# Performance work log

Measured on AMD Instinct MI355X. Metric: run time of the kernel, lower is better.

The kernel has to match this reference:

```python
import jax, jax.numpy as jnp
import numpy as np

N = 20000        # nodes
E = 320000       # edges
F_IN = 512       # feature_size
H = 512          # hidden_dim (z dim)
OUT = 1024       # output_size


def setup_inputs() -> dict:
    key = jax.random.key(0)
    ks = jax.random.split(key, 24)
    p = lambda k, shape: jax.random.normal(k, shape, jnp.float32) * 0.02
    return {
        "x": jax.random.normal(ks[0], (N, F_IN), jnp.float32),
        "edge_index": jax.random.randint(ks[1], (2, E), 0, N),
        "edge_weight": jax.random.uniform(ks[2], (E,), dtype=jnp.float32),
        "beta": jnp.float32(1.0),
        "y_target": jax.random.uniform(ks[3], (1,), dtype=jnp.float32),
        "eps": jax.random.normal(ks[4], (N, H), jnp.float32),
        # GCNConv weights (in_dim, out_dim) + bias
        "W1": p(ks[5], (F_IN, 1024)), "b1": jnp.zeros((1024,), jnp.float32),
        "W2": p(ks[6], (1024, 512)), "b2": jnp.zeros((512,), jnp.float32),
        "W3": p(ks[7], (512, 256)),  "b3": jnp.zeros((256,), jnp.float32),
        # VAE heads
        "Wmu": p(ks[8], (256, H)),  "bmu": jnp.zeros((H,), jnp.float32),
        "Wlv": p(ks[9], (256, H)),  "blv": jnp.zeros((H,), jnp.float32),
        # decoder MLP: (2H+1) -> (2H+1) -> OUT
        "Wd1": p(ks[10], (2 * H + 1, 2 * H + 1)), "bd1": jnp.zeros((2 * H + 1,), jnp.float32),
        "Wd2": p(ks[11], (2 * H + 1, OUT)),       "bd2": jnp.zeros((OUT,), jnp.float32),
    }


def gcn_conv(x, W, b, src, dst, ew):
    # PyG GCNConv: add self-loops (weight 1), symmetric deg normalization,
    # aggregate normalized neighbor messages of x @ W, then add bias.
    xw = x @ W                                             # [N, out]
    deg = jax.ops.segment_sum(ew, dst, num_segments=N) + 1.0
    dinv = jax.lax.rsqrt(deg)                              # [N]
    norm = dinv[src] * ew * dinv[dst]                      # [E]
    agg = jax.ops.segment_sum(norm[:, None] * xw[src], dst, num_segments=N)
    return agg + (dinv * dinv)[:, None] * xw + b


def l2norm(x):
    n = jnp.sqrt(jnp.sum(x * x, axis=1, keepdims=True))
    return x / jnp.maximum(n, 1e-12)


def reference(x, edge_index, edge_weight, beta, y_target, eps,
              W1, b1, W2, b2, W3, b3, Wmu, bmu, Wlv, blv, Wd1, bd1, Wd2, bd2):
    src, dst = edge_index[0], edge_index[1]
    h = jax.nn.relu(l2norm(gcn_conv(x, W1, b1, src, dst, edge_weight)))
    h = jax.nn.relu(l2norm(gcn_conv(h, W2, b2, src, dst, edge_weight)))
    h = jax.nn.relu(l2norm(gcn_conv(h, W3, b3, src, dst, edge_weight)))
    mu = h @ Wmu + bmu                                     # [N, H]
    logvar = h @ Wlv + blv                                 # [N, H]
    # reparameterize(mu, beta * logvar) with eps ~ 0.01 * N(0,1)
    std = jnp.exp(0.5 * beta * logvar)
    z = mu + (0.01 * eps) * std                            # [N, H]
    out1 = jnp.max(z, axis=0, keepdims=True)               # global max pool [1, H]
    out2 = jnp.mean(z, axis=0, keepdims=True)              # global mean pool [1, H]
    reduce_z = jnp.concatenate([out1, out2, y_target[:, None]], axis=-1)  # [1, 2H+1]
    hdec = jax.nn.relu(reduce_z @ Wd1 + bd1)
    recon_x = jax.nn.sigmoid(hdec @ Wd2 + bd2)             # [1, OUT]
    return (recon_x, mu, logvar)
```

## Files before the change

### kernel.cpp

```cpp
#include <hip/hip_runtime.h>

#define NN 20000
#define EE 320000
#define MPAD 20096
#define MTILES 157
#define DKB 128
#define DCH 9

typedef unsigned short u16;
typedef unsigned int u32;
typedef __attribute__((ext_vector_type(8))) short short8;
typedef __attribute__((ext_vector_type(4))) float f32x4;

__device__ inline float bf16lo(u32 u) { return __uint_as_float(u << 16); }
__device__ inline float bf16hi(u32 u) { return __uint_as_float(u & 0xffff0000u); }
__device__ inline u16 f2b(float f) {
  u32 u = __float_as_uint(f);
  u += 0x7fffu + ((u >> 16) & 1u);
  return (u16)(u >> 16);
}
__device__ inline u32 pack2(float a, float b) {
  return (u32)f2b(a) | ((u32)f2b(b) << 16);
}

__device__ inline void gload16(const void* g, void* l) {
  __builtin_amdgcn_global_load_lds(
      (const __attribute__((address_space(1))) void*)g,
      (__attribute__((address_space(3))) void*)l, 16, 0, 0);
}

__device__ inline int xcd_ord(int wg, int nwg) {
  int q = nwg >> 3, r = nwg & 7;
  int xcd = wg & 7, k = wg >> 3;
  return xcd * q + min(xcd, r) + k;
}

__global__ void k_zeroi(int* __restrict__ p, int n) {
  int i = blockIdx.x * blockDim.x + threadIdx.x;
  if (i < n) p[i] = 0;
}

__global__ void k_f2b2(const float* __restrict__ in, u16* __restrict__ out, int npairs) {
  for (int i = blockIdx.x * blockDim.x + threadIdx.x; i < npairs; i += gridDim.x * blockDim.x) {
    float2 v = *(const float2*)(in + 2 * i);
    ((u32*)out)[i] = pack2(v.x, v.y);
  }
}

__global__ void k_wt_all(const float* __restrict__ W1, const float* __restrict__ W2,
                         const float* __restrict__ W3, const float* __restrict__ Wmu,
                         const float* __restrict__ Wlv,
                         u16* __restrict__ T1, u16* __restrict__ T2,
                         u16* __restrict__ T3, u16* __restrict__ Tmu,
                         u16* __restrict__ Tlv) {
  int b = blockIdx.x;
  const float* W; u16* T; int K, N;
  if (b < 2048)      { W = W1;  T = T1;  K = 512;  N = 1024; }
  else if (b < 4096) { W = W2;  T = T2;  K = 1024; N = 512;  b -= 2048; }
  else if (b < 4608) { W = W3;  T = T3;  K = 512;  N = 256;  b -= 4096; }
  else if (b < 5120) { W = Wmu; T = Tmu; K = 256;  N = 512;  b -= 4608; }
  else               { W = Wlv; T = Tlv; K = 256;  N = 512;  b -= 5120; }
  int kb = K >> 8;
  int n = b / kb;
  int k = (b % kb) * 256 + threadIdx.x;
  T[(size_t)n * K + k] = f2b(W[(size_t)k * N + n]);
}

__global__ void k_count(const int* __restrict__ ei, int* __restrict__ counts) {
  int e = blockIdx.x * blockDim.x + threadIdx.x;
  if (e < EE) atomicAdd(counts + ei[EE + e], 1);
}

__global__ __launch_bounds__(256)
void k_scan(const int* __restrict__ counts, int* __restrict__ rowptr, int* __restrict__ cursor) {
  const int CHUNK = (NN + 255) / 256;
  int t = threadIdx.x;
  int lo = t * CHUNK, hi = min(lo + CHUNK, NN);
  int s = 0;
  for (int i = lo; i < hi; ++i) s += counts[i];
  __shared__ int tsum[256];
  tsum[t] = s;
  __syncthreads();
  if (t == 0) {
    int run = 0;
    for (int i = 0; i < 256; ++i) { int v = tsum[i]; tsum[i] = run; run += v; }
  }
  __syncthreads();
  int run = tsum[t];
  for (int i = lo; i < hi; ++i) {
    rowptr[i] = run;
    cursor[i] = run;
    run += counts[i];
  }
  if (t == 255) rowptr[NN] = EE;
}

__global__ void k_fill(const int* __restrict__ ei, const float* __restrict__ ew,
                       int* __restrict__ cursor, int* __restrict__ colsrc,
                       float* __restrict__ ecw) {
  int e = blockIdx.x * blockDim.x + threadIdx.x;
  if (e < EE) {
    int d = ei[EE + e];
    int pos = atomicAdd(cursor + d, 1);
    colsrc[pos] = ei[e];
    ecw[pos] = ew[e];
  }
}

__global__ void k_degcsr(const int* __restrict__ rowptr, const float* __restrict__ ecw,
                         float* __restrict__ dinv, float* __restrict__ dinv2) {
  int i = blockIdx.x * blockDim.x + threadIdx.x;
  if (i < NN) {
    float s = 0.f;
    for (int e = rowptr[i]; e < rowptr[i + 1]; ++e) s += ecw[e];
    float d = s + 1.0f;
    dinv[i] = rsqrtf(d);
    dinv2[i] = 1.0f / d;
  }
}

template <bool STORE_BF16, bool HAS_BIAS>
__global__ __launch_bounds__(256)
void k_mfma(const u16* __restrict__ A, const u16* __restrict__ BT,
            const float* __restrict__ bias, void* __restrict__ C,
            int M, int K, int N) {
  __shared__ u16 Asm[2][128 * 32];
  __shared__ u16 Bsm[2][128 * 32];
  const int tid = threadIdx.x;
  const int ntn = N >> 7;
  int ord = xcd_ord(blockIdx.x, gridDim.x);
  const int m0 = (ord / ntn) * 128;
  const int n0 = (ord % ntn) * 128;
  const int lane = tid & 63;
  const int wave = tid >> 6;
  const int wm = (wave >> 1) * 64;
  const int wn = (wave & 1) * 64;
  const int qm = lane & 15;
  const int quad = lane >> 4;

  f32x4 acc[4][4];
#pragma unroll
  for (int i = 0; i < 4; ++i)
#pragma unroll
    for (int j = 0; j < 4; ++j) acc[i][j] = (f32x4){0.f, 0.f, 0.f, 0.f};

  const int row_s = tid >> 2, kc_s = (tid & 3) * 8;

#pragma unroll
  for (int h = 0; h < 2; ++h) {
    int row = h * 64 + row_s;
    gload16(A + (size_t)(m0 + row) * K + kc_s, Asm[0] + row * 32 + kc_s);
    gload16(BT + (size_t)(n0 + row) * K + kc_s, Bsm[0] + row * 32 + kc_s);
  }
  __syncthreads();

  const int nk = K >> 5;
  int cur = 0;
  for (int t = 0; t < nk; ++t) {
    if (t + 1 < nk) {
      int k1 = (t + 1) * 32;
#pragma unroll
      for (int h = 0; h < 2; ++h) {
        int row = h * 64 + row_s;
        gload16(A + (size_t)(m0 + row) * K + k1 + kc_s, Asm[cur ^ 1] + row * 32 + kc_s);
        gload16(BT + (size_t)(n0 + row) * K + k1 + kc_s, Bsm[cur ^ 1] + row * 32 + kc_s);
      }
    }
    short8 af[4], bfr[4];
#pragma unroll
    for (int i = 0; i < 4; ++i)
      af[i] = *(const short8*)(Asm[cur] + (wm + i * 16 + qm) * 32 + quad * 8);
#pragma unroll
    for (int j = 0; j < 4; ++j)
      bfr[j] = *(const short8*)(Bsm[cur] + (wn + j * 16 + qm) * 32 + quad * 8);
#pragma unroll
    for (int i = 0; i < 4; ++i)
#pragma unroll
      for (int j = 0; j < 4; ++j)
        acc[i][j] = __builtin_amdgcn_mfma_f32_16x16x32_bf16(af[i], bfr[j], acc[i][j], 0, 0, 0);
    if (t + 1 < nk) {
      __syncthreads();
      cur ^= 1;
    }
  }

#pragma unroll
  for (int i = 0; i < 4; ++i) {
#pragma unroll
    for (int r = 0; r < 4; ++r) {
      int row = m0 + wm + i * 16 + quad * 4 + r;
      if (row >= M) continue;
#pragma unroll
      for (int j = 0; j < 4; ++j) {
        int col = n0 + wn + j * 16 + qm;
        float v = acc[i][j][r];
        if (HAS_BIAS) v += bias[col];
        if (STORE_BF16) ((u16*)C)[(size_t)row * N + col] = f2b(v);
        else ((float*)C)[(size_t)row * N + col] = v;
      }
    }
  }
}

__global__ __launch_bounds__(256, 3)
void k_heads(const u16* __restrict__ A, const u16* __restrict__ BmuT,
             const u16* __restrict__ BlvT, const float* __restrict__ bmu,
             const float* __restrict__ blv, const float* __restrict__ eps,
             const float* __restrict__ beta_p, float* __restrict__ mu_out,
             float* __restrict__ lv_out, float* __restrict__ pmax,
             float* __restrict__ psum) {
  const int K = 256;
  __shared__ float smemf[4352];
  u16* Asm = (u16*)smemf;
  u16* Bmu = (u16*)((char*)smemf + 8192);
  u16* Blv = (u16*)((char*)smemf + 12288);
  float* stmu = smemf;
  float* stlv = smemf + 32 * 68;
  const int tid = threadIdx.x;
  int ord = xcd_ord(blockIdx.x, gridDim.x);
  const int mt = ord >> 3;
  const int m0 = mt * 128;
  const int n0 = (ord & 7) * 64;
  const int lane = tid & 63;
  const int wave = tid >> 6;
  const int wm = (wave >> 1) * 64;
  const int wn = (wave & 1) * 32;
  const int qm = lane & 15;
  const int quad = lane >> 4;

  f32x4 am[4][2], al[4][2];
#pragma unroll
  for (int i = 0; i < 4; ++i)
#pragma unroll
    for (int j = 0; j < 2; ++j) {
      am[i][j] = (f32x4){0.f, 0.f, 0.f, 0.f};
      al[i][j] = (f32x4){0.f, 0.f, 0.f, 0.f};
    }

  for (int k0 = 0; k0 < K; k0 += 32) {
#pragma unroll
    for (int h = 0; h < 2; ++h) {
      int c = h * 256 + tid;
      int row = c >> 2, kc = c & 3;
      gload16(A + (size_t)(m0 + row) * K + k0 + kc * 8, Asm + c * 8);
    }
    {
      int row = tid >> 2, kc = tid & 3;
      gload16(BmuT + (size_t)(n0 + row) * K + k0 + kc * 8, Bmu + tid * 8);
      gload16(BlvT + (size_t)(n0 + row) * K + k0 + kc * 8, Blv + tid * 8);
    }
    __syncthreads();
    short8 af[4], bm[2], bl[2];
#pragma unroll
    for (int i = 0; i < 4; ++i)
      af[i] = *(const short8*)(Asm + (wm + i * 16 + qm) * 32 + quad * 8);
#pragma unroll
    for (int j = 0; j < 2; ++j) {
      bm[j] = *(const short8*)(Bmu + (wn + j * 16 + qm) * 32 + quad * 8);
      bl[j] = *(const short8*)(Blv + (wn + j * 16 + qm) * 32 + quad * 8);
    }
#pragma unroll
    for (int i = 0; i < 4; ++i)
#pragma unroll
      for (int j = 0; j < 2; ++j) {
        am[i][j] = __builtin_amdgcn_mfma_f32_16x16x32_bf16(af[i], bm[j], am[i][j], 0, 0, 0);
        al[i][j] = __builtin_amdgcn_mfma_f32_16x16x32_bf16(af[i], bl[j], al[i][j], 0, 0, 0);
      }
    __syncthreads();
  }

  const float beta = beta_p[0];
  float biasm[2], biasl[2];
#pragma unroll
  for (int j = 0; j < 2; ++j) {
    int col = n0 + wn + j * 16 + qm;
    biasm[j] = bmu[col];
    biasl[j] = blv[col];
  }

  float zmax[8], zsum[8];
#pragma unroll
  for (int q = 0; q < 8; ++q) { zmax[q] = -3.4e38f; zsum[q] = 0.f; }
  const int lrow_r = tid >> 3;
  const int colb = (tid & 7) * 8;

  for (int c = 0; c < 4; ++c) {
    __syncthreads();
    if ((wave >> 1) == (c >> 1)) {
      int ibase = (c & 1) * 2;
#pragma unroll
      for (int ii = 0; ii < 2; ++ii) {
        int i = ibase + ii;
#pragma unroll
        for (int j = 0; j < 2; ++j) {
          int lcol = wn + j * 16 + qm;
#pragma unroll
          for (int r = 0; r < 4; ++r) {
            int lr = ii * 16 + quad * 4 + r;
            stmu[lr * 68 + lcol] = am[i][j][r] + biasm[j];
            stlv[lr * 68 + lcol] = al[i][j][r] + biasl[j];
          }
        }
      }
    }
    __syncthreads();
    int grow = m0 + c * 32 + lrow_r;
    if (grow < NN) {
#pragma unroll
      for (int q4 = 0; q4 < 2; ++q4) {
        int lcol = colb + q4 * 4;
        float4 m4 = *(float4*)(stmu + lrow_r * 68 + lcol);
        float4 l4 = *(float4*)(stlv + lrow_r * 68 + lcol);
        size_t gidx = (size_t)grow * 512 + n0 + lcol;
        float4 e4 = *(const float4*)(eps + gidx);
        *(float4*)(mu_out + gidx) = m4;
        *(float4*)(lv_out + gidx) = l4;
        float z0 = m4.x + 0.01f * e4.x * expf(0.5f * beta * l4.x);
        float z1 = m4.y + 0.01f * e4.y * expf(0.5f * beta * l4.y);
        float z2 = m4.z + 0.01f * e4.z * expf(0.5f * beta * l4.z);
        float z3 = m4.w + 0.01f * e4.w * expf(0.5f * beta * l4.w);
        zmax[q4 * 4 + 0] = fmaxf(zmax[q4 * 4 + 0], z0); zsum[q4 * 4 + 0] += z0;
        zmax[q4 * 4 + 1] = fmaxf(zmax[q4 * 4 + 1], z1); zsum[q4 * 4 + 1] += z1;
        zmax[q4 * 4 + 2] = fmaxf(zmax[q4 * 4 + 2], z2); zsum[q4 * 4 + 2] += z2;
        zmax[q4 * 4 + 3] = fmaxf(zmax[q4 * 4 + 3], z3); zsum[q4 * 4 + 3] += z3;
      }
    }
  }

  __syncthreads();
  float* rbuf = smemf;
#pragma unroll
  for (int q = 0; q < 8; ++q) {
    rbuf[tid * 16 + q] = zmax[q];
    rbuf[tid * 16 + 8 + q] = zsum[q];
  }
  __syncthreads();
  if (tid < 64) {
    int g = tid >> 3, o = tid & 7;
    float m = -3.4e38f, s = 0.f;
    for (int k = 0; k < 32; ++k) {
      int src = (k * 8 + g) * 16;
      m = fmaxf(m, rbuf[src + o]);
      s += rbuf[src + 8 + o];
    }
    pmax[(size_t)mt * 512 + n0 + tid] = m;
    psum[(size_t)mt * 512 + n0 + tid] = s;
  }
}

__global__ void k_zred(const float* __restrict__ pmax, const float* __restrict__ psum,
                       const float* __restrict__ yt, float* __restrict__ rz) {
  int col = threadIdx.x;
  float m = -3.4e38f, s = 0.f;
  for (int c = 0; c < MTILES; ++c) {
    m = fmaxf(m, pmax[(size_t)c * 512 + col]);
    s += psum[(size_t)c * 512 + col];
  }
  rz[col] = m;
  rz[512 + col] = s / (float)NN;
  if (col == 0) rz[1024] = yt[0];
}

template <int NT, bool PRE>
__global__ __launch_bounds__(NT)
void k_gatherv(const int* __restrict__ rowptr, const int* __restrict__ colsrc,
               const float* __restrict__ ecw, const float* __restrict__ dinv,
               const float* __restrict__ dinv2, const u16* __restrict__ xw,
               const float* __restrict__ bias, u16* __restrict__ h) {
  const int O = 4 * NT;
  const int row = blockIdx.x;
  const int tid = threadIdx.x;
  const float dv = dinv[row], dv2 = dinv2[row];
  uint2 u = ((const uint2*)(xw + (size_t)row * O))[tid];
  float a0 = dv2 * bf16lo(u.x), a1 = dv2 * bf16hi(u.x);
  float a2 = dv2 * bf16lo(u.y), a3 = dv2 * bf16hi(u.y);
  if (!PRE) {
    a0 += bias[4 * tid];     a1 += bias[4 * tid + 1];
    a2 += bias[4 * tid + 2]; a3 += bias[4 * tid + 3];
  }
  float c0 = 0.f, c1 = 0.f, c2 = 0.f, c3 = 0.f;

  __shared__ int s_src[NT];
  __shared__ float s_w[NT];
  const int e0 = rowptr[row], e1 = rowptr[row + 1];
  for (int base = e0; base < e1; base += NT) {
    int cnt = min(NT, e1 - base);
    __syncthreads();
    if (tid < cnt) {
      int s = colsrc[base + tid];
      s_src[tid] = s;
      s_w[tid] = dinv[s] * ecw[base + tid] * dv;
    }
    __syncthreads();
    int e = 0;
    for (; e + 2 <= cnt; e += 2) {
      float w0 = s_w[e], w1 = s_w[e + 1];
      uint2 v0 = ((const uint2*)(xw + (size_t)s_src[e] * O))[tid];
      uint2 v1 = ((const uint2*)(xw + (size_t)s_src[e + 1] * O))[tid];
      a0 += w0 * bf16lo(v0.x); a1 += w0 * bf16hi(v0.x);
      a2 += w0 * bf16lo(v0.y); a3 += w0 * bf16hi(v0.y);
      c0 += w1 * bf16lo(v1.x); c1 += w1 * bf16hi(v1.x);
      c2 += w1 * bf16lo(v1.y); c3 += w1 * bf16hi(v1.y);
    }
    if (e < cnt) {
      float w = s_w[e];
      uint2 v = ((const uint2*)(xw + (size_t)s_src[e] * O))[tid];
      a0 += w * bf16lo(v.x); a1 += w * bf16hi(v.x);
      a2 += w * bf16lo(v.y); a3 += w * bf16hi(v.y);
    }
  }
  a0 += c0; a1 += c1; a2 += c2; a3 += c3;

  if (PRE) {
    uint2 o; o.x = pack2(a0, a1); o.y = pack2(a2, a3);
    ((uint2*)(h + (size_t)row * O))[tid] = o;
    return;
  }
  float ss = a0 * a0 + a1 * a1 + a2 * a2 + a3 * a3;
#pragma unroll
  for (int off = 32; off > 0; off >>= 1) ss += __shfl_down(ss, off, 64);
  __shared__ float red[(NT + 63) / 64];
  __shared__ float s_scale;
  if ((tid & 63) == 0) red[tid >> 6] = ss;
  __syncthreads();
  if (tid == 0) {
    float t = 0.f;
#pragma unroll
    for (int i = 0; i < (NT + 63) / 64; ++i) t += red[i];
    s_scale = 1.0f / fmaxf(sqrtf(t), 1e-12f);
  }
  __syncthreads();
  float sc = s_scale;
  uint2 o;
  o.x = pack2(fmaxf(a0 * sc, 0.f), fmaxf(a1 * sc, 0.f));
  o.y = pack2(fmaxf(a2 * sc, 0.f), fmaxf(a3 * sc, 0.f));
  ((uint2*)(h + (size_t)row * O))[tid] = o;
}

__global__ __launch_bounds__(256)
void k_l2relu(const u16* __restrict__ t, u16* __restrict__ h) {
  const int row = blockIdx.x;
  const int tid = threadIdx.x;
  const u32* tr = (const u32*)(t + (size_t)row * 1024);
  u32 u0 = tr[tid], u1 = tr[256 + tid];
  float a0 = bf16lo(u0), a1 = bf16hi(u0), a2 = bf16lo(u1), a3 = bf16hi(u1);
  float ss = a0 * a0 + a1 * a1 + a2 * a2 + a3 * a3;
#pragma unroll
  for (int off = 32; off > 0; off >>= 1) ss += __shfl_down(ss, off, 64);
  __shared__ float red[4];
  __shared__ float s_scale;
  if ((tid & 63) == 0) red[tid >> 6] = ss;
  __syncthreads();
  if (tid == 0) {
    float s = red[0] + red[1] + red[2] + red[3];
    s_scale = 1.0f / fmaxf(sqrtf(s), 1e-12f);
  }
  __syncthreads();
  float sc = s_scale;
  u32* hr = (u32*)(h + (size_t)row * 1024);
  hr[tid]       = pack2(fmaxf(a0 * sc, 0.f), fmaxf(a1 * sc, 0.f));
  hr[256 + tid] = pack2(fmaxf(a2 * sc, 0.f), fmaxf(a3 * sc, 0.f));
}

__global__ __launch_bounds__(256)
void k_dec_partial(const float* __restrict__ v, const float* __restrict__ W,
                   float* __restrict__ partial, int Kdim, int Ndim) {
  int b = blockIdx.x;
  int lo = b * DCH;
  float rv[DCH];
#pragma unroll
  for (int j = 0; j < DCH; ++j) rv[j] = (lo + j < Kdim) ? v[lo + j] : 0.f;
  for (int n = threadIdx.x; n < Ndim; n += 256) {
    float s = 0.f;
#pragma unroll
    for (int j = 0; j < DCH; ++j)
      if (lo + j < Kdim) s += rv[j] * W[(size_t)(lo + j) * Ndim + n];
    partial[(size_t)b * Ndim + n] = s;
  }
}

template <int ACT>
__global__ __launch_bounds__(256)
void k_dec_combine(const float* __restrict__ partial, const float* __restrict__ bias,
                   float* __restrict__ out, int Ndim) {
  int n = blockIdx.x * 256 + threadIdx.x;
  if (n >= Ndim) return;
  float s = bias[n];
  for (int b = 0; b < DKB; ++b) s += partial[(size_t)b * Ndim + n];
  out[n] = (ACT == 0) ? fmaxf(s, 0.f) : 1.0f / (1.0f + expf(-s));
}

extern "C" void kernel_launch(void* const* d_in, const int* in_sizes, int n_in,
                              void* d_out, int out_size, void* d_ws, size_t ws_size,
                              hipStream_t stream) {
  const float* x    = (const float*)d_in[0];
  const int*   ei   = (const int*)d_in[1];
  const float* ew   = (const float*)d_in[2];
  const float* beta = (const float*)d_in[3];
  const float* yt   = (const float*)d_in[4];
  const float* eps  = (const float*)d_in[5];
  const float* W1   = (const float*)d_in[6];  const float* b1  = (const float*)d_in[7];
  const float* W2   = (const float*)d_in[8];  const float* b2  = (const float*)d_in[9];
  const float* W3   = (const float*)d_in[10]; const float* b3  = (const float*)d_in[11];
  const float* Wmu  = (const float*)d_in[12]; const float* bmu = (const float*)d_in[13];
  const float* Wlv  = (const float*)d_in[14]; const float* blv = (const float*)d_in[15];
  const float* Wd1  = (const float*)d_in[16]; const float* bd1 = (const float*)d_in[17];
  const float* Wd2  = (const float*)d_in[18]; const float* bd2 = (const float*)d_in[19];

  char* wsb = (char*)d_ws;
  size_t off = 0;
  auto alloc_f = [&](size_t n) { float* p = (float*)(wsb + off); off += ((n * sizeof(float) + 15) & ~(size_t)15); return p; };
  auto alloc_i = [&](size_t n) { int* p = (int*)(wsb + off); off += ((n * sizeof(int) + 15) & ~(size_t)15); return p; };
  auto alloc_h = [&](size_t n) { u16* p = (u16*)(wsb + off); off += ((n * 2 + 15) & ~(size_t)15); return p; };

  int* counts  = alloc_i(NN);
  int* rowptr  = alloc_i(NN + 1);
  int* cursor  = alloc_i(NN);
  int* colsrc  = alloc_i(EE);
  float* ecw   = alloc_f(EE);
  float* dinv  = alloc_f(NN);
  float* din2  = alloc_f(NN);
  float* pmax  = alloc_f((size_t)MTILES * 512);
  float* psum  = alloc_f((size_t)MTILES * 512);
  float* rz    = alloc_f(1028);
  float* hdec  = alloc_f(1028);
  float* part1 = alloc_f((size_t)DKB * 1025);
  float* part2 = alloc_f((size_t)DKB * 1024);
  u16* W1T  = alloc_h(1024 * 512);
  u16* W2T  = alloc_h(512 * 1024);
  u16* W3T  = alloc_h(256 * 512);
  u16* WmuT = alloc_h(512 * 256);
  u16* WlvT = alloc_h(512 * 256);
  u16* xb   = alloc_h((size_t)MPAD * 512);
  u16* aggx = alloc_h((size_t)MPAD * 512);
  u16* bufT = alloc_h((size_t)MPAD * 1024);
  u16* bufH = alloc_h((size_t)MPAD * 1024);
  u16* h2   = alloc_h((size_t)MPAD * 512);
  u16* h3   = xb;
  u16* z2   = bufT;
  u16* z3   = bufH;

  float* out_f  = (float*)d_out;
  float* mu_out = out_f + 1024;
  float* lv_out = out_f + 1024 + (size_t)NN * 512;

  const int MT = MTILES;

  k_f2b2<<<4096, 256, 0, stream>>>(x, xb, NN * 512 / 2);
  k_wt_all<<<5632, 256, 0, stream>>>(W1, W2, W3, Wmu, Wlv, W1T, W2T, W3T, WmuT, WlvT);

  k_zeroi<<<(NN + 255) / 256, 256, 0, stream>>>(counts, NN);
  k_count<<<(EE + 255) / 256, 256, 0, stream>>>(ei, counts);
  k_scan<<<1, 256, 0, stream>>>(counts, rowptr, cursor);
  k_fill<<<(EE + 255) / 256, 256, 0, stream>>>(ei, ew, cursor, colsrc, ecw);
  k_degcsr<<<(NN + 255) / 256, 256, 0, stream>>>(rowptr, ecw, dinv, din2);

  k_gatherv<128, true><<<NN, 128, 0, stream>>>(rowptr, colsrc, ecw, dinv, din2, xb, nullptr, aggx);
  k_mfma<true, true><<<MT * 8, 256, 0, stream>>>(aggx, W1T, b1, bufT, NN, 512, 1024);
  k_l2relu<<<NN, 256, 0, stream>>>(bufT, bufH);

  k_mfma<true, false><<<MT * 4, 256, 0, stream>>>(bufH, W2T, nullptr, z2, NN, 1024, 512);
  k_gatherv<128, false><<<NN, 128, 0, stream>>>(rowptr, colsrc, ecw, dinv, din2, z2, b2, h2);

  k_mfma<true, false><<<MT * 2, 256, 0, stream>>>(h2, W3T, nullptr, z3, NN, 512, 256);
  k_gatherv<64, false><<<NN, 64, 0, stream>>>(rowptr, colsrc, ecw, dinv, din2, z3, b3, h3);

  k_heads<<<MT * 8, 256, 0, stream>>>(h3, WmuT, WlvT, bmu, blv, eps, beta,
                                      mu_out, lv_out, pmax, psum);
  k_zred<<<1, 512, 0, stream>>>(pmax, psum, yt, rz);

  k_dec_partial<<<DKB, 256, 0, stream>>>(rz, Wd1, part1, 1025, 1025);
  k_dec_combine<0><<<5, 256, 0, stream>>>(part1, bd1, hdec, 1025);
  k_dec_partial<<<DKB, 256, 0, stream>>>(hdec, Wd2, part2, 1025, 1024);
  k_dec_combine<1><<<4, 256, 0, stream>>>(part2, bd2, out_f, 1024);
}
```

Baseline: 641.1 us.

## Double-buffer LDS tiles in heads GEMM and prefetch eps before epilogue

The heads kernel now uses two LDS buffers for the A, Wmu and Wlv tiles. The next K-slice is loaded while MFMAs run on the current one, which removes one barrier per iteration. The eps values for the epilogue are also loaded into registers right after the GEMM, so their latency overlaps the LDS staging. The cost is LDS growing from about 17 KB to 32 KB per block and more live registers, which may reduce occupancy under the 3-blocks launch bound.

```diff
diff --git a/kernel.cpp b/kernel.cpp
--- a/kernel.cpp
+++ b/kernel.cpp
@@ -210,12 +210,13 @@
              float* __restrict__ lv_out, float* __restrict__ pmax,
              float* __restrict__ psum) {
   const int K = 256;
-  __shared__ float smemf[4352];
-  u16* Asm = (u16*)smemf;
-  u16* Bmu = (u16*)((char*)smemf + 8192);
-  u16* Blv = (u16*)((char*)smemf + 12288);
-  float* stmu = smemf;
-  float* stlv = smemf + 32 * 68;
+  __shared__ char smem[32768];
+  u16* AsmD[2] = {(u16*)smem, (u16*)(smem + 8192)};
+  u16* BmuD[2] = {(u16*)(smem + 16384), (u16*)(smem + 20480)};
+  u16* BlvD[2] = {(u16*)(smem + 24576), (u16*)(smem + 28672)};
+  float* stmu = (float*)smem;
+  float* stlv = (float*)(smem + 8704);
+  float* rbuf = (float*)smem;
   const int tid = threadIdx.x;
   int ord = xcd_ord(blockIdx.x, gridDim.x);
   const int mt = ord >> 3;
@@ -237,27 +238,36 @@
       al[i][j] = (f32x4){0.f, 0.f, 0.f, 0.f};
     }
 
-  for (int k0 = 0; k0 < K; k0 += 32) {
-#pragma unroll
-    for (int h = 0; h < 2; ++h) {
-      int c = h * 256 + tid;
-      int row = c >> 2, kc = c & 3;
-      gload16(A + (size_t)(m0 + row) * K + k0 + kc * 8, Asm + c * 8);
-    }
-    {
-      int row = tid >> 2, kc = tid & 3;
-      gload16(BmuT + (size_t)(n0 + row) * K + k0 + kc * 8, Bmu + tid * 8);
-      gload16(BlvT + (size_t)(n0 + row) * K + k0 + kc * 8, Blv + tid * 8);
-    }
-    __syncthreads();
+  const int rowA = tid >> 2, kcA = (tid & 3) * 8;
+#pragma unroll
+  for (int h = 0; h < 2; ++h) {
+    int row = h * 64 + rowA;
+    gload16(A + (size_t)(m0 + row) * K + kcA, AsmD[0] + row * 32 + kcA);
+  }
+  gload16(BmuT + (size_t)(n0 + rowA) * K + kcA, BmuD[0] + tid * 8);
+  gload16(BlvT + (size_t)(n0 + rowA) * K + kcA, BlvD[0] + tid * 8);
+  __syncthreads();
+
+  int cur = 0;
+  for (int t = 0; t < 8; ++t) {
+    if (t < 7) {
+      int k1 = (t + 1) * 32;
+#pragma unroll
+      for (int h = 0; h < 2; ++h) {
+        int row = h * 64 + rowA;
+        gload16(A + (size_t)(m0 + row) * K + k1 + kcA, AsmD[cur ^ 1] + row * 32 + kcA);
+      }
+      gload16(BmuT + (size_t)(n0 + rowA) * K + k1 + kcA, BmuD[cur ^ 1] + tid * 8);
+      gload16(BlvT + (size_t)(n0 + rowA) * K + k1 + kcA, BlvD[cur ^ 1] + tid * 8);
+    }
     short8 af[4], bm[2], bl[2];
 #pragma unroll
     for (int i = 0; i < 4; ++i)
-      af[i] = *(const short8*)(Asm + (wm + i * 16 + qm) * 32 + quad * 8);
+      af[i] = *(const short8*)(AsmD[cur] + (wm + i * 16 + qm) * 32 + quad * 8);
 #pragma unroll
     for (int j = 0; j < 2; ++j) {
-      bm[j] = *(const short8*)(Bmu + (wn + j * 16 + qm) * 32 + quad * 8);
-      bl[j] = *(const short8*)(Blv + (wn + j * 16 + qm) * 32 + quad * 8);
+      bm[j] = *(const short8*)(BmuD[cur] + (wn + j * 16 + qm) * 32 + quad * 8);
+      bl[j] = *(const short8*)(BlvD[cur] + (wn + j * 16 + qm) * 32 + quad * 8);
     }
 #pragma unroll
     for (int i = 0; i < 4; ++i)
@@ -266,7 +276,10 @@
         am[i][j] = __builtin_amdgcn_mfma_f32_16x16x32_bf16(af[i], bm[j], am[i][j], 0, 0, 0);
         al[i][j] = __builtin_amdgcn_mfma_f32_16x16x32_bf16(af[i], bl[j], al[i][j], 0, 0, 0);
       }
-    __syncthreads();
+    if (t < 7) {
+      __syncthreads();
+      cur ^= 1;
+    }
   }
 
   const float beta = beta_p[0];
@@ -278,12 +291,27 @@
     biasl[j] = blv[col];
   }
 
-  float zmax[8], zsum[8];
-#pragma unroll
-  for (int q = 0; q < 8; ++q) { zmax[q] = -3.4e38f; zsum[q] = 0.f; }
   const int lrow_r = tid >> 3;
   const int colb = (tid & 7) * 8;
 
+  float4 e4pre[4][2];
+#pragma unroll
+  for (int c = 0; c < 4; ++c) {
+    int grow = m0 + c * 32 + lrow_r;
+    if (grow < NN) {
+#pragma unroll
+      for (int q4 = 0; q4 < 2; ++q4) {
+        size_t gidx = (size_t)grow * 512 + n0 + colb + q4 * 4;
+        e4pre[c][q4] = *(const float4*)(eps + gidx);
+      }
+    }
+  }
+
+  float zmax[8], zsum[8];
+#pragma unroll
+  for (int q = 0; q < 8; ++q) { zmax[q] = -3.4e38f; zsum[q] = 0.f; }
+
+#pragma unroll
   for (int c = 0; c < 4; ++c) {
     __syncthreads();
     if ((wave >> 1) == (c >> 1)) {
@@ -312,7 +340,7 @@
         float4 m4 = *(float4*)(stmu + lrow_r * 68 + lcol);
         float4 l4 = *(float4*)(stlv + lrow_r * 68 + lcol);
         size_t gidx = (size_t)grow * 512 + n0 + lcol;
-        float4 e4 = *(const float4*)(eps + gidx);
+        float4 e4 = e4pre[c][q4];
         *(float4*)(mu_out + gidx) = m4;
         *(float4*)(lv_out + gidx) = l4;
         float z0 = m4.x + 0.01f * e4.x * expf(0.5f * beta * l4.x);
@@ -328,7 +356,6 @@
   }
 
   __syncthreads();
-  float* rbuf = smemf;
 #pragma unroll
   for (int q = 0; q < 8; ++q) {
     rbuf[tid * 16 + q] = zmax[q];
```

Result: no change. 637.5 us (-0.6%).
